# Performance work log

Hardware: AMD Instinct MI355X
Metric: run time of the kernel (lower is better)

The kernel has to match this reference:

```python
import jax, jax.numpy as jnp
import numpy as np

B, C, H, W = 2, 64, 256, 256
K, DG, PAD = 3, 8, 1
KK = K * K
CG = C // DG


def _conv(x, w, b):
    y = jax.lax.conv_general_dilated(x, w, (1, 1), [(PAD, PAD), (PAD, PAD)],
                                     dimension_numbers=('NCHW', 'OIHW', 'NCHW'))
    return y + b[None, :, None, None]


def _bilinear_one(img, y, x):
    # img: (CG, H, W); y, x: (KK, H, W) float sampling coords; zero-padded bilinear
    y0 = jnp.floor(y)
    x0 = jnp.floor(x)
    wy = y - y0
    wx = x - x0

    def tap(yi, xi, wgt):
        valid = (yi >= 0) & (yi < H) & (xi >= 0) & (xi < W)
        yc = jnp.clip(yi, 0, H - 1).astype(jnp.int32)
        xc = jnp.clip(xi, 0, W - 1).astype(jnp.int32)
        v = img[:, yc, xc]  # (CG, KK, H, W)
        return v * (wgt * valid)[None]

    return (tap(y0, x0, (1 - wy) * (1 - wx)) +
            tap(y0, x0 + 1, (1 - wy) * wx) +
            tap(y0 + 1, x0, wy * (1 - wx)) +
            tap(y0 + 1, x0 + 1, wy * wx))


_sample = jax.vmap(jax.vmap(_bilinear_one))  # over batch, then deform group


def setup_inputs() -> dict:
    key = jax.random.key(0)
    ks = jax.random.split(key, 7)
    n_off = 2 * KK * DG
    n_msk = KK * DG
    bound = 1.0 / np.sqrt(C * K * K)  # kaiming_uniform(a=sqrt(5)) bound
    return {
        'ref': jax.random.normal(ks[0], (B, C, H, W), jnp.float32),
        'neighbour': jax.random.normal(ks[1], (B, C, H, W), jnp.float32),
        'off_w': jax.random.normal(ks[2], (n_off, 2 * C, K, K), jnp.float32) * 0.01,
        'off_b': jnp.zeros((n_off,), jnp.float32),
        'mask_w': jax.random.normal(ks[3], (n_msk, 2 * C, K, K), jnp.float32) * 0.01,
        'mask_b': jnp.zeros((n_msk,), jnp.float32),
        'weight': jax.random.uniform(ks[4], (C, C, K, K), jnp.float32, -bound, bound),
        'bias': jnp.zeros((C,), jnp.float32),
    }


def reference(ref, neighbour, off_w, off_b, mask_w, mask_b, weight, bias):
    concat = jnp.concatenate([ref, neighbour], axis=1)            # (B, 2C, H, W)
    offset = _conv(concat, off_w, off_b)                          # (B, 2*DG*KK, H, W)
    mask = jax.nn.sigmoid(_conv(concat, mask_w, mask_b))          # (B, DG*KK, H, W)

    off = offset.reshape(B, DG, KK, 2, H, W)
    dy, dx = off[:, :, :, 0], off[:, :, :, 1]

    ki, kj = jnp.meshgrid(jnp.arange(K), jnp.arange(K), indexing='ij')
    ki = ki.reshape(KK).astype(jnp.float32)
    kj = kj.reshape(KK).astype(jnp.float32)
    base_y = jnp.arange(H, dtype=jnp.float32)[None, :, None] - PAD + ki[:, None, None]
    base_x = jnp.arange(W, dtype=jnp.float32)[None, None, :] - PAD + kj[:, None, None]
    ys = dy + base_y                                              # (B, DG, KK, H, W)
    xs = dx + base_x

    img_g = neighbour.reshape(B, DG, CG, H, W)
    sampled = _sample(img_g, ys, xs)                              # (B, DG, CG, KK, H, W)
    sampled = sampled * mask.reshape(B, DG, 1, KK, H, W)

    wr = weight.reshape(C, DG, CG, KK)
    out = jnp.einsum('bgckhw,ogck->bohw', sampled, wr)
    return out + bias[None, :, None, None]
```

## Files before the change

kernel.cpp:

```cpp
#include <hip/hip_runtime.h>
#include <hip/hip_fp16.h>
#include <cstdint>
#include <cstddef>

#define B_ 2
#define C_ 64
#define H_ 256
#define W_ 256
#define HW_ (H_*W_)
#define DG_ 8
#define CG_ 8
#define KK_ 9
#define NOFF_ 144
#define NMSK_ 72
#define NTOT_ 216
#define KRED_ 1152
#define XPH_ 258

typedef __bf16 bf16x8 __attribute__((ext_vector_type(8)));
typedef _Float16 half8 __attribute__((ext_vector_type(8)));
typedef short  short8 __attribute__((ext_vector_type(8)));
typedef float  f32x4  __attribute__((ext_vector_type(4)));

__device__ __forceinline__ short f2bf(float f) {
    union { float f; uint32_t u; } a; a.f = f;
    uint32_t u = a.u;
    uint32_t r = (u + 0x7fffu + ((u >> 16) & 1u)) >> 16;
    return (short)r;
}

typedef __attribute__((address_space(1))) const unsigned int g_u32;
typedef __attribute__((address_space(3))) unsigned int l_u32;
__device__ __forceinline__ void gl_lds16(const void* g, void* l) {
    __builtin_amdgcn_global_load_lds((g_u32*)g, (l_u32*)l, 16, 0, 0);
}

__global__ void wtrans2_kernel(const float* __restrict__ off_w,
                               const float* __restrict__ msk_w,
                               short* __restrict__ Bw) {
    int idx = blockIdx.x * 256 + threadIdx.x;
    int s    = idx >> 13;
    int rem  = idx & 8191;
    int n    = rem >> 5;
    int slot = (rem >> 3) & 3;
    int j    = rem & 7;
    int q    = slot ^ ((n >> 1) & 3);
    int c4   = s / 9;
    int tap  = s - c4 * 9;
    int ch   = c4 * 32 + q * 8 + j;
    float v = 0.f;
    if (n < NOFF_)      v = off_w[(size_t)n * KRED_ + ch * 9 + tap];
    else if (n < NTOT_) v = msk_w[(size_t)(n - NOFF_) * KRED_ + ch * 9 + tap];
    Bw[idx] = f2bf(v);
}

__global__ void wtrans3_kernel(const float* __restrict__ weight,
                               short* __restrict__ Bw3) {
    int idx = blockIdx.x * 256 + threadIdx.x;
    int kc   = idx >> 11;
    int rem  = idx & 2047;
    int n    = rem >> 5;
    int slot = (rem >> 3) & 3;
    int j    = rem & 7;
    int q    = slot ^ ((n >> 1) & 3);
    int k    = kc >> 1;
    int g    = ((kc & 1) << 2) + q;
    int ci   = g * 8 + j;
    union { _Float16 h; short s; } cv;
    cv.h = (_Float16)weight[((size_t)n * 64 + ci) * 9 + k];
    Bw3[idx] = cv.s;
}

__global__ void pack_xp2(const float* __restrict__ ref,
                         const float* __restrict__ nbr,
                         short* __restrict__ xp,
                         short* __restrict__ nbf) {
    const int by = blockIdx.x;
    const int b  = by / XPH_;
    const int yi = by - b * XPH_;
    const int c4 = blockIdx.y;
    const int yg = yi - 1;
    const float* base = (c4 < 2 ? ref : nbr) + ((size_t)b * 64 + (c4 & 1) * 32) * HW_;
    short* rowbase = xp + (((size_t)(b * 4 + c4) * XPH_ + yi) * XPH_) * 32;
    for (int xi = threadIdx.x; xi < XPH_; xi += 256) {
        const int xg = xi - 1;
        const bool valid = ((unsigned)yg < H_) && ((unsigned)xg < W_);
        short* dst = rowbase + (size_t)xi * 32;
        const int sig = (xi >> 1) & 3;
        #pragma unroll
        for (int q = 0; q < 4; ++q) {
            float v[8];
            if (valid) {
                const float* p = base + (size_t)(q * 8) * HW_ + (size_t)yg * W_ + xg;
                #pragma unroll
                for (int j = 0; j < 8; ++j) v[j] = p[(size_t)j * HW_];
            } else {
                #pragma unroll
                for (int j = 0; j < 8; ++j) v[j] = 0.f;
            }
            short8 o;
            #pragma unroll
            for (int j = 0; j < 8; ++j) o[j] = f2bf(v[j]);
            *reinterpret_cast<short8*>(dst + ((q ^ sig) * 8)) = o;
            if (c4 >= 2 && valid) {
                const int g = (c4 - 2) * 4 + q;
                union { half8 h8; short8 s8; } u;
                #pragma unroll
                for (int j = 0; j < 8; ++j) u.h8[j] = (_Float16)v[j];
                *reinterpret_cast<short8*>(
                    nbf + ((size_t)(b * 8 + g) * HW_ + (size_t)yg * W_ + xg) * 8) = u.s8;
            }
        }
    }
}

struct OffV { float dy, dx, mm; };
struct GathV { half8 c00, c01, c10, c11; float a00, a01, a10, a11; };

__global__ __launch_bounds__(512, 4) void fused_conv_apply(
    const short* __restrict__ xp, const short* __restrict__ Bw,
    const float* __restrict__ off_b, const float* __restrict__ msk_b,
    const short* __restrict__ nbf, const short* __restrict__ Bw3,
    const float* __restrict__ bias, float* __restrict__ out)
{
    __shared__ __align__(16) short AsBuf[2][4608];
    __shared__ __align__(16) short offmsk[NTOT_ * 128];

    const int tid  = threadIdx.x;
    const int lane = tid & 63;
    const int wid  = tid >> 6;
    const int wm   = wid & 1;
    const int wn   = wid >> 1;
    const int col     = lane & 15;
    const int quad    = lane >> 4;
    const int rowbase = quad * 4;

    const int bid = blockIdx.x;
    const int wg  = (bid & 7) * 128 + (bid >> 3);
    const int m0 = wg << 7;
    const int b  = m0 >> 16;
    const int h  = (m0 >> 8) & 255;
    const int w0 = m0 & 255;

    {
        int bOff[4];
        #pragma unroll
        for (int nt = 0; nt < 4; ++nt) {
            int n = wn * 64 + nt * 16 + col;
            bOff[nt] = (n * 4 + (quad ^ ((n >> 1) & 3))) * 8;
        }
        int pxv[4];
        #pragma unroll
        for (int mt = 0; mt < 4; ++mt) pxv[mt] = wm * 64 + mt * 16 + col;

        f32x4 acc[4][4];
        #pragma unroll
        for (int i = 0; i < 4; ++i)
            #pragma unroll
            for (int j = 0; j < 4; ++j) acc[i][j] = f32x4{0.f, 0.f, 0.f, 0.f};

        auto stageA = [&](int win, int bb) {
            const int c4s = win / 3;
            const int dys = win - c4s * 3;
            const short* sA = xp + (((size_t)(b * 4 + c4s) * XPH_ + (h + dys)) * XPH_
                                    + w0) * 32;
            char* dA = (char*)&AsBuf[bb][0];
            gl_lds16(sA + (size_t)tid * 8, dA + wid * 1024);
            if (tid < 32) gl_lds16(sA + (size_t)(512 + tid) * 8, dA + 8192);
        };

        stageA(0, 0);
        __syncthreads();

        #pragma unroll 1
        for (int win = 0; win < 12; ++win) {
            const int bb = win & 1;
            if (win < 11) stageA(win + 1, bb ^ 1);
            const short* AsC = &AsBuf[bb][0];

            #pragma unroll
            for (int dx = 0; dx < 3; ++dx) {
                const int s = win * 3 + dx;
                const short* bp = Bw + ((size_t)s << 13);

                bf16x8 bv[4];
                #pragma unroll
                for (int nt = 0; nt < 4; ++nt)
                    bv[nt] = *reinterpret_cast<const bf16x8*>(bp + bOff[nt]);

                bf16x8 af[4];
                #pragma unroll
                for (int mt = 0; mt < 4; ++mt) {
                    const int px = pxv[mt] + dx;
                    af[mt] = *reinterpret_cast<const bf16x8*>(
                        &AsC[(px * 4 + (quad ^ ((px >> 1) & 3))) * 8]);
                }

                #pragma unroll
                for (int mt = 0; mt < 4; ++mt)
                    #pragma unroll
                    for (int nt = 0; nt < 4; ++nt)
                        acc[mt][nt] = __builtin_amdgcn_mfma_f32_16x16x32_bf16(
                            af[mt], bv[nt], acc[mt][nt], 0, 0, 0);
            }
            __syncthreads();
        }

        #pragma unroll
        for (int mt = 0; mt < 4; ++mt) {
            const int p4 = wm * 64 + mt * 16 + rowbase;
            #pragma unroll
            for (int nt = 0; nt < 4; ++nt) {
                const int n = wn * 64 + nt * 16 + col;
                if (n >= NTOT_) continue;
                const bool is_off = (n < NOFF_);
                const float bia = is_off ? off_b[n] : msk_b[n - NOFF_];
                union { uint2 u; __half hx[4]; } pk;
                #pragma unroll
                for (int rr = 0; rr < 4; ++rr) {
                    float v = acc[mt][nt][rr] + bia;
                    if (!is_off) v = 1.f / (1.f + __expf(-v));
                    pk.hx[rr] = __float2half(v);
                }
                const int byt = n * 256 + ((2 * p4) ^ ((n & 7) << 4));
                *(uint2*)((char*)offmsk + byt) = pk.u;
            }
        }
    }
    __syncthreads();

    {
        const int p     = tid & 127;
        const int q     = tid >> 7;
        const int w     = w0 + p;
        const int slotW = q ^ ((p >> 1) & 3);

        auto ldsOff = [&](int n, int pp) -> float {
            const int byt = n * 256 + ((2 * pp) ^ ((n & 7) << 4));
            return __half2float(*reinterpret_cast<const __half*>(
                (const char*)offmsk + byt));
        };
        auto loadOffs = [&](int kc) -> OffV {
            const int k = kc >> 1;
            const int g = ((kc & 1) << 2) + q;
            OffV o;
            o.dy = ldsOff(g * 18 + 2 * k,     p);
            o.dx = ldsOff(g * 18 + 2 * k + 1, p);
            o.mm = ldsOff(NOFF_ + g * 9 + k,  p);
            return o;
        };

        auto issueGather = [&](int kc, OffV o) -> GathV {
            const int k  = kc >> 1;
            const int g  = ((kc & 1) << 2) + q;
            const int ky = k / 3;
            const int kx = k - ky * 3;
            float ys = (float)(h - 1 + ky) + o.dy;
            float xs = (float)(w - 1 + kx) + o.dx;
            float y0f = floorf(ys), x0f = floorf(xs);
            float wy = ys - y0f, wx = xs - x0f;
            int y0 = (int)y0f, x0 = (int)x0f;
            int y1 = y0 + 1, x1 = x0 + 1;
            int yc0 = min(max(y0, 0), H_-1), yc1 = min(max(y1, 0), H_-1);
            float wy0v = (1.f - wy) * (((unsigned)y0 < H_) ? o.mm : 0.f);
            float wy1v = wy * (((unsigned)y1 < H_) ? o.mm : 0.f);
            int xb = min(max(x0, 0), W_-2);
            float wx0v = (((unsigned)x0 < W_) ? (1.f - wx) : 0.f);
            float wx1v = (((unsigned)x1 < W_) ? wx : 0.f);
            float sx0 = (x0 == xb) ? wx0v : ((x1 == xb) ? wx1v : 0.f);
            float sx1 = (x1 == xb + 1) ? wx1v : ((x0 == xb + 1) ? wx0v : 0.f);
            GathV gv;
            gv.a00 = wy0v * sx0; gv.a01 = wy0v * sx1;
            gv.a10 = wy1v * sx0; gv.a11 = wy1v * sx1;
            const short* nb = nbf + (size_t)(b * 8 + g) * HW_ * 8;
            const short* r0 = nb + ((size_t)yc0 * W_ + xb) * 8;
            const short* r1 = nb + ((size_t)yc1 * W_ + xb) * 8;
            gv.c00 = *reinterpret_cast<const half8*>(r0);
            gv.c01 = *reinterpret_cast<const half8*>(r0 + 8);
            gv.c10 = *reinterpret_cast<const half8*>(r1);
            gv.c11 = *reinterpret_cast<const half8*>(r1 + 8);
            return gv;
        };

        auto combineWrite = [&](int kc, const GathV& gv) {
            union { half8 h8; short8 s8; } u;
            #pragma unroll
            for (int c = 0; c < CG_; ++c) {
                float v = gv.a00 * (float)gv.c00[c] + gv.a01 * (float)gv.c01[c]
                        + gv.a10 * (float)gv.c10[c] + gv.a11 * (float)gv.c11[c];
                u.h8[c] = (_Float16)v;
            }
            *reinterpret_cast<short8*>(&AsBuf[kc & 1][(p * 4 + slotW) * 8]) = u.s8;
        };

        const int nB = wn * 16 + col;
        const short* bPtr = Bw3 + ((nB * 4 + (quad ^ ((nB >> 1) & 3))) << 3);

        f32x4 acc2[4];
        #pragma unroll
        for (int mt = 0; mt < 4; ++mt) acc2[mt] = f32x4{0.f, 0.f, 0.f, 0.f};

        {
            OffV o0 = loadOffs(0);
            GathV g0 = issueGather(0, o0);
            combineWrite(0, g0);
        }
        GathV G = issueGather(1, loadOffs(1));
        __syncthreads();

        #pragma unroll 1
        for (int kc = 0; kc < 18; ++kc) {
            const int bb = kc & 1;
            const short* AsC = &AsBuf[bb][0];

            half8 bv = *reinterpret_cast<const half8*>(bPtr + ((size_t)kc << 11));
            half8 af[4];
            #pragma unroll
            for (int mt = 0; mt < 4; ++mt) {
                const int px = wm * 64 + mt * 16 + col;
                af[mt] = *reinterpret_cast<const half8*>(
                    &AsC[(px * 4 + (quad ^ ((px >> 1) & 3))) * 8]);
            }

            if (kc + 1 < 18) combineWrite(kc + 1, G);
            if (kc + 2 < 18) G = issueGather(kc + 2, loadOffs(kc + 2));

            #pragma unroll
            for (int mt = 0; mt < 4; ++mt)
                acc2[mt] = __builtin_amdgcn_mfma_f32_16x16x32_f16(af[mt], bv, acc2[mt], 0, 0, 0);

            __syncthreads();
        }

        const int o = wn * 16 + col;
        const float bo = bias[o];
        float* op = out + ((size_t)b * C_ + o) * HW_ + (size_t)h * W_ + w0;
        #pragma unroll
        for (int mt = 0; mt < 4; ++mt) {
            const int px = wm * 64 + mt * 16 + quad * 4;
            float4 st = make_float4(acc2[mt][0] + bo, acc2[mt][1] + bo,
                                    acc2[mt][2] + bo, acc2[mt][3] + bo);
            *(float4*)(op + px) = st;
        }
    }
}

extern "C" void kernel_launch(void* const* d_in, const int* in_sizes, int n_in,
                              void* d_out, int out_size, void* d_ws, size_t ws_size,
                              hipStream_t stream) {
    const float* ref    = (const float*)d_in[0];
    const float* nbr    = (const float*)d_in[1];
    const float* off_w  = (const float*)d_in[2];
    const float* off_b  = (const float*)d_in[3];
    const float* msk_w  = (const float*)d_in[4];
    const float* msk_b  = (const float*)d_in[5];
    const float* weight = (const float*)d_in[6];
    const float* bias   = (const float*)d_in[7];
    float* out = (float*)d_out;

    const size_t sz_Bw  = (size_t)36 * 256 * 32 * 2;
    const size_t sz_xp  = (size_t)B_ * 4 * XPH_ * XPH_ * 32 * 2
                          + 16384;
    const size_t sz_Bw3 = (size_t)18 * 64 * 32 * 2;

    char* ws = (char*)d_ws;
    short* Bw  = (short*)ws;
    short* xp  = (short*)(ws + sz_Bw);
    short* Bw3 = (short*)(ws + sz_Bw + sz_xp);
    short* nbf = (short*)(ws + sz_Bw + sz_xp + sz_Bw3);

    wtrans2_kernel<<<1152, 256, 0, stream>>>(off_w, msk_w, Bw);
    wtrans3_kernel<<<144, 256, 0, stream>>>(weight, Bw3);
    pack_xp2<<<dim3(B_ * XPH_, 4), 256, 0, stream>>>(ref, nbr, xp, nbf);
    fused_conv_apply<<<1024, 512, 0, stream>>>(xp, Bw, off_b, msk_b,
                                               nbf, Bw3, bias, out);
}
```

Baseline: 252.9 us.

## Merge prep kernels, deepen gather prefetch, raise MFMA wave priority

Folds the two weight-transform kernels and the input-packing kernel into one launch with block-range dispatch, removing two kernel launches and their gaps. In the deformable apply loop, gathers are now issued three steps ahead using two alternating register sets instead of two steps ahead with one, to hide more gather latency. MFMA sections in both GEMM phases are wrapped in s_setprio to favour waves issuing matrix ops. Holding two gather sets in registers raises register pressure, which may hurt occupancy under the 512x4 launch bounds.

```diff
diff --git a/kernel.cpp b/kernel.cpp
--- a/kernel.cpp
+++ b/kernel.cpp
@@ -35,82 +35,86 @@
     __builtin_amdgcn_global_load_lds((g_u32*)g, (l_u32*)l, 16, 0, 0);
 }
 
-__global__ void wtrans2_kernel(const float* __restrict__ off_w,
-                               const float* __restrict__ msk_w,
-                               short* __restrict__ Bw) {
-    int idx = blockIdx.x * 256 + threadIdx.x;
-    int s    = idx >> 13;
-    int rem  = idx & 8191;
-    int n    = rem >> 5;
-    int slot = (rem >> 3) & 3;
-    int j    = rem & 7;
-    int q    = slot ^ ((n >> 1) & 3);
-    int c4   = s / 9;
-    int tap  = s - c4 * 9;
-    int ch   = c4 * 32 + q * 8 + j;
-    float v = 0.f;
-    if (n < NOFF_)      v = off_w[(size_t)n * KRED_ + ch * 9 + tap];
-    else if (n < NTOT_) v = msk_w[(size_t)(n - NOFF_) * KRED_ + ch * 9 + tap];
-    Bw[idx] = f2bf(v);
-}
-
-__global__ void wtrans3_kernel(const float* __restrict__ weight,
-                               short* __restrict__ Bw3) {
-    int idx = blockIdx.x * 256 + threadIdx.x;
-    int kc   = idx >> 11;
-    int rem  = idx & 2047;
-    int n    = rem >> 5;
-    int slot = (rem >> 3) & 3;
-    int j    = rem & 7;
-    int q    = slot ^ ((n >> 1) & 3);
-    int k    = kc >> 1;
-    int g    = ((kc & 1) << 2) + q;
-    int ci   = g * 8 + j;
-    union { _Float16 h; short s; } cv;
-    cv.h = (_Float16)weight[((size_t)n * 64 + ci) * 9 + k];
-    Bw3[idx] = cv.s;
-}
-
-__global__ void pack_xp2(const float* __restrict__ ref,
-                         const float* __restrict__ nbr,
-                         short* __restrict__ xp,
-                         short* __restrict__ nbf) {
-    const int by = blockIdx.x;
-    const int b  = by / XPH_;
-    const int yi = by - b * XPH_;
-    const int c4 = blockIdx.y;
-    const int yg = yi - 1;
-    const float* base = (c4 < 2 ? ref : nbr) + ((size_t)b * 64 + (c4 & 1) * 32) * HW_;
-    short* rowbase = xp + (((size_t)(b * 4 + c4) * XPH_ + yi) * XPH_) * 32;
-    for (int xi = threadIdx.x; xi < XPH_; xi += 256) {
-        const int xg = xi - 1;
-        const bool valid = ((unsigned)yg < H_) && ((unsigned)xg < W_);
-        short* dst = rowbase + (size_t)xi * 32;
-        const int sig = (xi >> 1) & 3;
-        #pragma unroll
-        for (int q = 0; q < 4; ++q) {
-            float v[8];
-            if (valid) {
-                const float* p = base + (size_t)(q * 8) * HW_ + (size_t)yg * W_ + xg;
-                #pragma unroll
-                for (int j = 0; j < 8; ++j) v[j] = p[(size_t)j * HW_];
-            } else {
-                #pragma unroll
-                for (int j = 0; j < 8; ++j) v[j] = 0.f;
-            }
-            short8 o;
-            #pragma unroll
-            for (int j = 0; j < 8; ++j) o[j] = f2bf(v[j]);
-            *reinterpret_cast<short8*>(dst + ((q ^ sig) * 8)) = o;
-            if (c4 >= 2 && valid) {
-                const int g = (c4 - 2) * 4 + q;
-                union { half8 h8; short8 s8; } u;
-                #pragma unroll
-                for (int j = 0; j < 8; ++j) u.h8[j] = (_Float16)v[j];
-                *reinterpret_cast<short8*>(
-                    nbf + ((size_t)(b * 8 + g) * HW_ + (size_t)yg * W_ + xg) * 8) = u.s8;
-            }
-        }
+__global__ __launch_bounds__(256) void prep_all(
+    const float* __restrict__ ref, const float* __restrict__ nbr,
+    const float* __restrict__ off_w, const float* __restrict__ msk_w,
+    const float* __restrict__ weight,
+    short* __restrict__ xp, short* __restrict__ nbf,
+    short* __restrict__ Bw, short* __restrict__ Bw3)
+{
+    const int bid = blockIdx.x;
+    const int tid = threadIdx.x;
+
+    if (bid < 2064) {
+        const int by = bid >> 2;
+        const int c4 = bid & 3;
+        const int b  = by / XPH_;
+        const int yi = by - b * XPH_;
+        const int yg = yi - 1;
+        const float* base = (c4 < 2 ? ref : nbr)
+                            + ((size_t)b * 64 + (c4 & 1) * 32) * HW_;
+        short* rowbase = xp + (((size_t)(b * 4 + c4) * XPH_ + yi) * XPH_) * 32;
+        for (int xi = tid; xi < XPH_; xi += 256) {
+            const int xg = xi - 1;
+            const bool valid = ((unsigned)yg < H_) && ((unsigned)xg < W_);
+            short* dst = rowbase + (size_t)xi * 32;
+            const int sig = (xi >> 1) & 3;
+            #pragma unroll
+            for (int q = 0; q < 4; ++q) {
+                float v[8];
+                if (valid) {
+                    const float* p = base + (size_t)(q * 8) * HW_
+                                     + (size_t)yg * W_ + xg;
+                    #pragma unroll
+                    for (int j = 0; j < 8; ++j) v[j] = p[(size_t)j * HW_];
+                } else {
+                    #pragma unroll
+                    for (int j = 0; j < 8; ++j) v[j] = 0.f;
+                }
+                short8 o;
+                #pragma unroll
+                for (int j = 0; j < 8; ++j) o[j] = f2bf(v[j]);
+                *reinterpret_cast<short8*>(dst + ((q ^ sig) * 8)) = o;
+                if (c4 >= 2 && valid) {
+                    const int g = (c4 - 2) * 4 + q;
+                    union { half8 h8; short8 s8; } u;
+                    #pragma unroll
+                    for (int j = 0; j < 8; ++j) u.h8[j] = (_Float16)v[j];
+                    *reinterpret_cast<short8*>(
+                        nbf + ((size_t)(b * 8 + g) * HW_
+                               + (size_t)yg * W_ + xg) * 8) = u.s8;
+                }
+            }
+        }
+    } else if (bid < 3216) {
+        int idx = (bid - 2064) * 256 + tid;
+        int s    = idx >> 13;
+        int rem  = idx & 8191;
+        int n    = rem >> 5;
+        int slot = (rem >> 3) & 3;
+        int j    = rem & 7;
+        int q    = slot ^ ((n >> 1) & 3);
+        int c4   = s / 9;
+        int tap  = s - c4 * 9;
+        int ch   = c4 * 32 + q * 8 + j;
+        float v = 0.f;
+        if (n < NOFF_)      v = off_w[(size_t)n * KRED_ + ch * 9 + tap];
+        else if (n < NTOT_) v = msk_w[(size_t)(n - NOFF_) * KRED_ + ch * 9 + tap];
+        Bw[idx] = f2bf(v);
+    } else {
+        int idx = (bid - 3216) * 256 + tid;
+        int kc   = idx >> 11;
+        int rem  = idx & 2047;
+        int n    = rem >> 5;
+        int slot = (rem >> 3) & 3;
+        int j    = rem & 7;
+        int q    = slot ^ ((n >> 1) & 3);
+        int k    = kc >> 1;
+        int g    = ((kc & 1) << 2) + q;
+        int ci   = g * 8 + j;
+        union { _Float16 h; short s; } cv;
+        cv.h = (_Float16)weight[((size_t)n * 64 + ci) * 9 + k];
+        Bw3[idx] = cv.s;
     }
 }
 
@@ -196,12 +200,14 @@
                         &AsC[(px * 4 + (quad ^ ((px >> 1) & 3))) * 8]);
                 }
 
+                __builtin_amdgcn_s_setprio(1);
                 #pragma unroll
                 for (int mt = 0; mt < 4; ++mt)
                     #pragma unroll
                     for (int nt = 0; nt < 4; ++nt)
                         acc[mt][nt] = __builtin_amdgcn_mfma_f32_16x16x32_bf16(
                             af[mt], bv[nt], acc[mt][nt], 0, 0, 0);
+                __builtin_amdgcn_s_setprio(0);
             }
             __syncthreads();
         }
@@ -305,13 +311,12 @@
             GathV g0 = issueGather(0, o0);
             combineWrite(0, g0);
         }
-        GathV G = issueGather(1, loadOffs(1));
+        GathV GA = issueGather(1, loadOffs(1));
+        GathV GB = issueGather(2, loadOffs(2));
         __syncthreads();
 
-        #pragma unroll 1
-        for (int kc = 0; kc < 18; ++kc) {
-            const int bb = kc & 1;
-            const short* AsC = &AsBuf[bb][0];
+        auto bodyKC = [&](int kc, GathV& Gcur, GathV& Gnext) {
+            const short* AsC = &AsBuf[kc & 1][0];
 
             half8 bv = *reinterpret_cast<const half8*>(bPtr + ((size_t)kc << 11));
             half8 af[4];
@@ -322,14 +327,23 @@
                     &AsC[(px * 4 + (quad ^ ((px >> 1) & 3))) * 8]);
             }
 
-            if (kc + 1 < 18) combineWrite(kc + 1, G);
-            if (kc + 2 < 18) G = issueGather(kc + 2, loadOffs(kc + 2));
-
+            if (kc + 1 < 18) combineWrite(kc + 1, Gcur);
+            if (kc + 3 < 18) Gcur = issueGather(kc + 3, loadOffs(kc + 3));
+
+            __builtin_amdgcn_s_setprio(1);
             #pragma unroll
             for (int mt = 0; mt < 4; ++mt)
-                acc2[mt] = __builtin_amdgcn_mfma_f32_16x16x32_f16(af[mt], bv, acc2[mt], 0, 0, 0);
-
+                acc2[mt] = __builtin_amdgcn_mfma_f32_16x16x32_f16(
+                    af[mt], bv, acc2[mt], 0, 0, 0);
+            __builtin_amdgcn_s_setprio(0);
             __syncthreads();
+            (void)Gnext;
+        };
+
+        #pragma unroll 1
+        for (int kc2 = 0; kc2 < 18; kc2 += 2) {
+            bodyKC(kc2,     GA, GB);
+            bodyKC(kc2 + 1, GB, GA);
         }
 
         const int o = wn * 16 + col;
@@ -369,9 +383,8 @@
     short* Bw3 = (short*)(ws + sz_Bw + sz_xp);
     short* nbf = (short*)(ws + sz_Bw + sz_xp + sz_Bw3);
 
-    wtrans2_kernel<<<1152, 256, 0, stream>>>(off_w, msk_w, Bw);
-    wtrans3_kernel<<<144, 256, 0, stream>>>(weight, Bw3);
-    pack_xp2<<<dim3(B_ * XPH_, 4), 256, 0, stream>>>(ref, nbr, xp, nbf);
+    prep_all<<<3360, 256, 0, stream>>>(ref, nbr, off_w, msk_w, weight,
+                                       xp, nbf, Bw, Bw3);
     fused_conv_apply<<<1024, 512, 0, stream>>>(xp, Bw, off_b, msk_b,
                                                nbf, Bw3, bias, out);
 }
```

Result: no change. 248.2 us (-1.9%).
